# Kernel tuning notes

Hardware: AMD Instinct MI355X
Metric: run time of the kernel (lower is better)

## Reference

```python
import jax, jax.numpy as jnp
import numpy as np

N, IN_DIM, HID, E_DIM, E = 50000, 128, 256, 32, 400000
BN_INV = np.float32(1.0 / np.sqrt(1.0 + 1e-5))  # running_mean=0, running_var=1


def _lin_init(key, fan_in, fan_out):
    kw, kb = jax.random.split(key)
    s = 1.0 / np.sqrt(fan_in)
    W = jax.random.uniform(kw, (fan_in, fan_out), jnp.float32, -s, s)
    b = jax.random.uniform(kb, (fan_out,), jnp.float32, -s, s)
    return W, b


def setup_inputs() -> dict:
    key = jax.random.key(0)
    ks = jax.random.split(key, 12)
    x = jax.random.normal(ks[0], (N, IN_DIM), jnp.float32)
    edge_index = jax.random.randint(ks[1], (2, E), 0, N, jnp.int64)
    edge_attr = jax.random.normal(ks[2], (E, E_DIM), jnp.float32)
    Wn, bn_b = _lin_init(ks[3], IN_DIM, HID)
    We, be = _lin_init(ks[4], E_DIM, HID)
    Wa1, ba1 = _lin_init(ks[5], 2 * HID, HID)
    Wa2, ba2 = _lin_init(ks[6], HID, 1)
    W1, b1 = _lin_init(ks[7], HID, 2 * HID)
    W2, b2 = _lin_init(ks[8], 2 * HID, HID)
    gn = jnp.ones((HID,), jnp.float32); betan = jnp.zeros((HID,), jnp.float32)
    ge = jnp.ones((HID,), jnp.float32); betae = jnp.zeros((HID,), jnp.float32)
    gm = jnp.ones((2 * HID,), jnp.float32); betam = jnp.zeros((2 * HID,), jnp.float32)
    eps = jnp.zeros((1,), jnp.float32)
    return dict(x=x, edge_index=edge_index, edge_attr=edge_attr,
                Wn=Wn, bn_b=bn_b, gn=gn, betan=betan,
                We=We, be=be, ge=ge, betae=betae,
                Wa1=Wa1, ba1=ba1, Wa2=Wa2, ba2=ba2,
                W1=W1, b1=b1, gm=gm, betam=betam, W2=W2, b2=b2, eps=eps)


def _bn(h, g, b):
    # eval-mode BatchNorm1d with running_mean=0, running_var=1
    return h * (g * BN_INV) + b


def reference(x, edge_index, edge_attr, Wn, bn_b, gn, betan, We, be, ge, betae,
              Wa1, ba1, Wa2, ba2, W1, b1, gm, betam, W2, b2, eps):
    h = jax.nn.relu(_bn(x @ Wn + bn_b, gn, betan))           # [N, HID] node_encoder
    ef = jax.nn.relu(_bn(edge_attr @ We + be, ge, betae))    # [E, HID] edge_encoder
    row, col = edge_index[0], edge_index[1]
    ni = h[row]                                              # [E, HID]
    nj = h[col]                                              # [E, HID]
    att_in = jnp.concatenate([ni + ef, nj], axis=-1)         # [E, 2*HID]
    a = jnp.tanh(att_in @ Wa1 + ba1) @ Wa2 + ba2             # [E, 1]
    a = jax.nn.leaky_relu(a, 0.2)
    a = jax.nn.softmax(a, axis=0)                            # softmax over all edges
    msg = (nj + ef) * a                                      # [E, HID]
    agg = jnp.zeros_like(h).at[row].add(msg)                 # scatter-add
    out = (1.0 + eps) * h + agg
    mid = jax.nn.relu(_bn(out @ W1 + b1, gm, betam))         # MLP hidden [N, 2*HID]
    return mid @ W2 + b2                                     # [N, HID]
```

## Files before the change

kernel.cpp:

```cpp
#include <hip/hip_runtime.h>

typedef __attribute__((ext_vector_type(8))) short    s16x8;
typedef __attribute__((ext_vector_type(8))) unsigned short u16x8;
typedef __attribute__((ext_vector_type(4))) unsigned short u16x4;
typedef __attribute__((ext_vector_type(4))) float    f32x4;

#define BN_INV 0.9999950000374997f
#define MAXDEG 64
#define INV64  0.015625f

__device__ __forceinline__ unsigned short f2b(float f) {
    union { float f; unsigned u; } v; v.f = f;
    return (unsigned short)((v.u + 0x7FFFu + ((v.u >> 16) & 1u)) >> 16);
}
__device__ __forceinline__ float b2f(unsigned short b) {
    union { unsigned u; float f; } v; v.u = (unsigned)b << 16;
    return v.f;
}
__device__ __forceinline__ float fast_tanh(float x) {
    float e = __expf(-2.f * fabsf(x));
    float t = (1.f - e) / (1.f + e);
    return copysignf(t, x);
}

__global__ __launch_bounds__(256) void gemm_mfma(
    const void* __restrict__ Av, int lda, int a_f32,
    const unsigned short* __restrict__ BT, int ldb, int bsplit,
    float* __restrict__ Cf, unsigned short* __restrict__ Cb, int ldc,
    const float* __restrict__ bias, const float* __restrict__ gamma,
    const float* __restrict__ beta, int M, int K, int bnrelu)
{
    __shared__ unsigned short As[128 * 40];
    __shared__ unsigned short Bs[128 * 40];

    const int tid = threadIdx.x;
    const int row0 = blockIdx.y * 128;
    const int col0 = blockIdx.x * 128;
    const int w = tid >> 6, l = tid & 63;
    const int wr = (w >> 1) * 64;
    const int wc = (w & 1) * 64;
    const int srow = tid >> 1;
    const int shalf = (tid & 1) * 16;

    f32x4 acc[4][4];
    #pragma unroll
    for (int i = 0; i < 4; ++i)
        #pragma unroll
        for (int j = 0; j < 4; ++j)
            acc[i][j] = (f32x4){0.f, 0.f, 0.f, 0.f};

    const bool arow_ok = (row0 + srow) < M;
    const unsigned short* Ab = (const unsigned short*)Av + (size_t)(row0 + srow) * lda + shalf;
    const float*          Af = (const float*)Av          + (size_t)(row0 + srow) * lda + shalf;
    int bcol = col0 + srow, koff = 0;
    if (bsplit && col0 >= bsplit) { bcol -= bsplit; koff = bsplit; }
    const unsigned short* Bp = BT + (size_t)bcol * ldb + koff + shalf;

    const int lrow = (l >> 4) * 4;
    const int lcol = l & 15;
    const int kfrag = (l >> 4) * 8;

    for (int kt = 0; kt < K; kt += 32) {
        u16x8 av0 = {0, 0, 0, 0, 0, 0, 0, 0};
        u16x8 av1 = {0, 0, 0, 0, 0, 0, 0, 0};
        if (arow_ok) {
            if (a_f32) {
                float4 u0 = *(const float4*)(Af + kt);
                float4 u1 = *(const float4*)(Af + kt + 4);
                float4 u2 = *(const float4*)(Af + kt + 8);
                float4 u3 = *(const float4*)(Af + kt + 12);
                av0 = (u16x8){ f2b(u0.x), f2b(u0.y), f2b(u0.z), f2b(u0.w),
                               f2b(u1.x), f2b(u1.y), f2b(u1.z), f2b(u1.w) };
                av1 = (u16x8){ f2b(u2.x), f2b(u2.y), f2b(u2.z), f2b(u2.w),
                               f2b(u3.x), f2b(u3.y), f2b(u3.z), f2b(u3.w) };
            } else {
                av0 = *(const u16x8*)(Ab + kt);
                av1 = *(const u16x8*)(Ab + kt + 8);
            }
        }
        u16x8 bv0 = *(const u16x8*)(Bp + kt);
        u16x8 bv1 = *(const u16x8*)(Bp + kt + 8);
        *(u16x8*)&As[srow * 40 + shalf]     = av0;
        *(u16x8*)&As[srow * 40 + shalf + 8] = av1;
        *(u16x8*)&Bs[srow * 40 + shalf]     = bv0;
        *(u16x8*)&Bs[srow * 40 + shalf + 8] = bv1;
        __syncthreads();
        s16x8 af[4], bfr[4];
        #pragma unroll
        for (int i = 0; i < 4; ++i)
            af[i] = *(const s16x8*)&As[(wr + i * 16 + lcol) * 40 + kfrag];
        #pragma unroll
        for (int j = 0; j < 4; ++j)
            bfr[j] = *(const s16x8*)&Bs[(wc + j * 16 + lcol) * 40 + kfrag];
        #pragma unroll
        for (int i = 0; i < 4; ++i)
            #pragma unroll
            for (int j = 0; j < 4; ++j)
                acc[i][j] = __builtin_amdgcn_mfma_f32_16x16x32_bf16(
                    af[i], bfr[j], acc[i][j], 0, 0, 0);
        __syncthreads();
    }

    #pragma unroll
    for (int j = 0; j < 4; ++j) {
        const int col = col0 + wc + j * 16 + lcol;
        const float bi = bias ? bias[col] : 0.f;
        float g = 1.f, bt = 0.f;
        if (bnrelu) { g = gamma[col] * BN_INV; bt = beta[col]; }
        #pragma unroll
        for (int i = 0; i < 4; ++i) {
            const int r0 = row0 + wr + i * 16 + lrow;
            #pragma unroll
            for (int q = 0; q < 4; ++q) {
                const int rr = r0 + q;
                if (rr < M) {
                    float v = acc[i][j][q] + bi;
                    if (bnrelu) v = fmaxf(v * g + bt, 0.f);
                    if (Cf) Cf[(size_t)rr * ldc + col] = v;
                    if (Cb) Cb[(size_t)rr * ldc + col] = f2b(v);
                }
            }
        }
    }
}

__global__ __launch_bounds__(256) void fused_edge(
    const float* __restrict__ ea,
    const int* __restrict__ ei,
    const unsigned short* __restrict__ WeT,
    const unsigned char* __restrict__ Wa1T8,
    const unsigned short* __restrict__ HAB,
    const float* __restrict__ be, const float* __restrict__ ge,
    const float* __restrict__ betae, const float* __restrict__ ba1,
    const float* __restrict__ Wa2, const float* __restrict__ ba2,
    unsigned char* __restrict__ EF,
    float* __restrict__ es, float* __restrict__ Ssum, int E)
{
    __shared__ __align__(16) unsigned char smem[18432];
    unsigned short* As  = (unsigned short*)smem;
    unsigned char*  EFs = smem;
    int*   sIdx = (int*)(smem + 16384);
    float* sRed = (float*)(smem + 16896);

    const int tid = threadIdx.x;
    const int row0 = blockIdx.x * 64;
    const int w = tid >> 6, l = tid & 63;
    const int lgrp = l >> 4, lcol = l & 15;
    const int kfrag = lgrp * 8;
    const int wc = w * 64;

    {
        const int sr = tid >> 2, sk = (tid & 3) * 8;
        u16x8 av = {0, 0, 0, 0, 0, 0, 0, 0};
        if (row0 + sr < E) {
            const float* ap = ea + (size_t)(row0 + sr) * 32 + sk;
            float4 u0 = *(const float4*)ap, u1 = *(const float4*)(ap + 4);
            av = (u16x8){ f2b(u0.x), f2b(u0.y), f2b(u0.z), f2b(u0.w),
                          f2b(u1.x), f2b(u1.y), f2b(u1.z), f2b(u1.w) };
        }
        *(u16x8*)&As[sr * 40 + sk] = av;
        if (tid < 64)       sIdx[tid] = (row0 + tid < E) ? ei[row0 + tid] : 0;
        else if (tid < 128) sIdx[tid] = (row0 + tid - 64 < E) ? ei[E + row0 + tid - 64] : 0;
    }
    __syncthreads();

    f32x4 acc[4][4];
    #pragma unroll
    for (int i = 0; i < 4; ++i)
        #pragma unroll
        for (int j = 0; j < 4; ++j)
            acc[i][j] = (f32x4){0.f, 0.f, 0.f, 0.f};

    {
        s16x8 af[4], bfr[4];
        #pragma unroll
        for (int i = 0; i < 4; ++i)
            af[i] = *(const s16x8*)&WeT[(wc + i * 16 + lcol) * 32 + kfrag];
        #pragma unroll
        for (int j = 0; j < 4; ++j)
            bfr[j] = *(const s16x8*)&As[(j * 16 + lcol) * 40 + kfrag];
        #pragma unroll
        for (int i = 0; i < 4; ++i)
            #pragma unroll
            for (int j = 0; j < 4; ++j)
                acc[i][j] = __builtin_amdgcn_mfma_f32_16x16x32_bf16(
                    af[i], bfr[j], acc[i][j], 0, 0, 0);
    }
    __syncthreads();

    #pragma unroll
    for (int i = 0; i < 4; ++i) {
        const int ch0 = wc + i * 16 + lgrp * 4;
        float4 g4 = *(const float4*)(ge + ch0);
        float4 t4 = *(const float4*)(betae + ch0);
        float4 b4 = *(const float4*)(be + ch0);
        g4.x *= BN_INV; g4.y *= BN_INV; g4.z *= BN_INV; g4.w *= BN_INV;
        #pragma unroll
        for (int j = 0; j < 4; ++j) {
            const int edge = j * 16 + lcol;
            float v0 = fmaxf((acc[i][j][0] + b4.x) * g4.x + t4.x, 0.f);
            float v1 = fmaxf((acc[i][j][1] + b4.y) * g4.y + t4.y, 0.f);
            float v2 = fmaxf((acc[i][j][2] + b4.z) * g4.z + t4.z, 0.f);
            float v3 = fmaxf((acc[i][j][3] + b4.w) * g4.w + t4.w, 0.f);
            int pk = __builtin_amdgcn_cvt_pk_fp8_f32(v0, v1, 0, false);
            pk = __builtin_amdgcn_cvt_pk_fp8_f32(v2, v3, pk, true);
            *(unsigned*)&EFs[edge * 256 + ((((ch0 >> 3) ^ (edge & 7)) << 3) | (ch0 & 7))]
                = (unsigned)pk;
            acc[i][j] = (f32x4){0.f, 0.f, 0.f, 0.f};
        }
    }
    __syncthreads();

    for (int kt = 0; kt < 256; kt += 32) {
        long af8[4], bf8[4];
        const int kb = (kt + kfrag) >> 3;
        #pragma unroll
        for (int i = 0; i < 4; ++i) {
            const int edge = i * 16 + lcol;
            af8[i] = *(const long*)&EFs[edge * 256 + ((kb ^ (edge & 7)) << 3)];
        }
        #pragma unroll
        for (int j = 0; j < 4; ++j)
            bf8[j] = *(const long*)&Wa1T8[(size_t)(wc + j * 16 + lcol) * 256 + kt + kfrag];
        #pragma unroll
        for (int i = 0; i < 4; ++i)
            #pragma unroll
            for (int j = 0; j < 4; ++j)
                acc[i][j] = __builtin_amdgcn_mfma_f32_16x16x32_fp8_fp8(
                    af8[i], bf8[j], acc[i][j], 0, 0, 0);
    }

    {
        const int row = tid >> 2, cb = (tid & 3) * 64;
        if (row0 + row < E) {
            unsigned char* dst = EF + (size_t)(row0 + row) * 256 + cb;
            #pragma unroll
            for (int t2 = 0; t2 < 8; ++t2) {
                const int b = (cb >> 3) + t2;
                *(long*)(dst + t2 * 8)
                    = *(const long*)&EFs[row * 256 + ((b ^ (row & 7)) << 3)];
            }
        }
    }

    {
        int colv[4]; float ba1c[4], wa2c[4];
        #pragma unroll
        for (int j = 0; j < 4; ++j) {
            colv[j] = wc + j * 16 + lcol;
            ba1c[j] = ba1[colv[j]];
            wa2c[j] = Wa2[colv[j]];
        }
        #pragma unroll
        for (int i = 0; i < 4; ++i) {
            #pragma unroll
            for (int q = 0; q < 4; ++q) {
                const int row = i * 16 + lgrp * 4 + q;
                const unsigned short* hap = HAB + (size_t)sIdx[row] * 512;
                const unsigned short* hbp = HAB + (size_t)sIdx[64 + row] * 512 + 256;
                float s = 0.f;
                #pragma unroll
                for (int j = 0; j < 4; ++j) {
                    float t = fast_tanh(fmaf(acc[i][j][q], INV64,
                                             b2f(hap[colv[j]]) + b2f(hbp[colv[j]]) + ba1c[j]));
                    s += t * wa2c[j];
                }
                s += __shfl_xor(s, 1); s += __shfl_xor(s, 2);
                s += __shfl_xor(s, 4); s += __shfl_xor(s, 8);
                if (lcol == 0) sRed[row * 4 + w] = s;
            }
        }
    }
    __syncthreads();

    if (tid < 64) {
        const int ge = row0 + tid;
        float sv = sRed[tid * 4] + sRed[tid * 4 + 1]
                 + sRed[tid * 4 + 2] + sRed[tid * 4 + 3] + ba2[0];
        sv = sv > 0.f ? sv : 0.2f * sv;
        float ev = __expf(sv);
        float contrib = 0.f;
        if (ge < E) { es[ge] = ev; contrib = ev; }
        #pragma unroll
        for (int off = 32; off; off >>= 1) contrib += __shfl_xor(contrib, off);
        if (l == 0) atomicAdd(Ssum, contrib);
    }
}

__global__ __launch_bounds__(256) void fill_kernel(
    const int* __restrict__ ei, int* __restrict__ cnt, int* __restrict__ perm,
    int E)
{
    int e = blockIdx.x * 256 + threadIdx.x;
    const int stride = gridDim.x * 256;
    for (; e < E; e += stride) {
        const int r = ei[e];
        const int pos = atomicAdd(&cnt[r], 1);
        if (pos < MAXDEG) perm[(size_t)r * MAXDEG + pos] = e;
    }
}

__global__ __launch_bounds__(256) void gather_kernel(
    const int* __restrict__ ei, const unsigned char* __restrict__ EF,
    const unsigned short* __restrict__ h_bf, const float* __restrict__ es,
    const int* __restrict__ cnt, const int* __restrict__ perm,
    const float* __restrict__ eps, const float* __restrict__ Ssum,
    unsigned short* __restrict__ ob_bf, int N, int E)
{
    const int w = threadIdx.x >> 6, l = threadIdx.x & 63;
    const int r = blockIdx.x * 4 + w;
    if (r >= N) return;
    const int k0 = l * 4;

    const int deg = cnt[r] < MAXDEG ? cnt[r] : MAXDEG;
    const int pe = perm[(size_t)r * MAXDEG + l];
    const float esl = (l < deg) ? es[pe] : 0.f;
    const int   cl  = (l < deg) ? ei[E + pe] : 0;

    f32x4 acc = {0.f, 0.f, 0.f, 0.f};
    u16x4 hv_c = {0, 0, 0, 0}; int ef_c = 0; float es_c = 0.f;
    if (deg > 0) {
        const int e0 = __shfl(pe, 0), c0 = __shfl(cl, 0);
        es_c = __shfl(esl, 0);
        hv_c = *(const u16x4*)(h_bf + (size_t)c0 * 256 + k0);
        ef_c = *(const int*)(EF + (size_t)e0 * 256 + k0);
    }
    for (int p = 0; p < deg; ++p) {
        u16x4 hv_n = {0, 0, 0, 0}; int ef_n = 0; float es_n = 0.f;
        if (p + 1 < deg) {
            const int en = __shfl(pe, p + 1), cn = __shfl(cl, p + 1);
            es_n = __shfl(esl, p + 1);
            hv_n = *(const u16x4*)(h_bf + (size_t)cn * 256 + k0);
            ef_n = *(const int*)(EF + (size_t)en * 256 + k0);
        }
        acc[0] += es_c * (b2f(hv_c[0]) + __builtin_amdgcn_cvt_f32_fp8(ef_c, 0));
        acc[1] += es_c * (b2f(hv_c[1]) + __builtin_amdgcn_cvt_f32_fp8(ef_c, 1));
        acc[2] += es_c * (b2f(hv_c[2]) + __builtin_amdgcn_cvt_f32_fp8(ef_c, 2));
        acc[3] += es_c * (b2f(hv_c[3]) + __builtin_amdgcn_cvt_f32_fp8(ef_c, 3));
        hv_c = hv_n; ef_c = ef_n; es_c = es_n;
    }

    const float sc = 1.f + eps[0];
    const float invS = 1.f / Ssum[0];
    u16x4 hr = *(const u16x4*)(h_bf + (size_t)r * 256 + k0);
    u16x4 o = { f2b(sc * b2f(hr[0]) + acc[0] * invS),
                f2b(sc * b2f(hr[1]) + acc[1] * invS),
                f2b(sc * b2f(hr[2]) + acc[2] * invS),
                f2b(sc * b2f(hr[3]) + acc[3] * invS) };
    *(u16x4*)(ob_bf + (size_t)r * 256 + k0) = o;
}

__global__ __launch_bounds__(256) void prep_kernel(
    const float* __restrict__ Wn, const float* __restrict__ We,
    const float* __restrict__ Wa1, const float* __restrict__ W1,
    const float* __restrict__ W2,
    unsigned short* __restrict__ WnT, unsigned short* __restrict__ WeT,
    unsigned short* __restrict__ Wa1T, unsigned char* __restrict__ Wa1T8,
    unsigned short* __restrict__ W1T, unsigned short* __restrict__ W2T,
    int* __restrict__ cnt, float* __restrict__ Ssum, int N)
{
    const int b = blockIdx.x, t = threadIdx.x;
    { const int i = b * 256 + t; if (i < N) cnt[i] = 0; }
    if (b == 0 && t == 0) Ssum[0] = 0.f;
    if (b < 128) {
        WnT[t * 128 + b] = f2b(Wn[(size_t)b * 256 + t]);
    } else if (b < 160) {
        const int rr = b - 128;
        WeT[t * 32 + rr] = f2b(We[(size_t)rr * 256 + t]);
    } else if (b < 672) {
        const int rr = b - 160;
        const float v = Wa1[(size_t)rr * 256 + t];
        Wa1T[t * 512 + rr] = f2b(v);
        if (rr < 256) {
            int pk = __builtin_amdgcn_cvt_pk_fp8_f32(v * 64.f, 0.f, 0, false);
            Wa1T8[(size_t)t * 256 + rr] = (unsigned char)(pk & 0xFF);
        }
    } else if (b < 928) {
        const int rr = b - 672;
        W1T[(size_t)t * 256 + rr]         = f2b(W1[(size_t)rr * 512 + t]);
        W1T[(size_t)(t + 256) * 256 + rr] = f2b(W1[(size_t)rr * 512 + t + 256]);
    } else if (b < 1440) {
        const int rr = b - 928;
        W2T[(size_t)t * 512 + rr] = f2b(W2[(size_t)rr * 256 + t]);
    }
}

extern "C" void kernel_launch(void* const* d_in, const int* in_sizes, int n_in,
                              void* d_out, int out_size, void* d_ws, size_t ws_size,
                              hipStream_t stream)
{
    const float* x     = (const float*)d_in[0];
    const int*   ei    = (const int*)  d_in[1];
    const float* eattr = (const float*)d_in[2];
    const float* Wn    = (const float*)d_in[3];
    const float* bnb   = (const float*)d_in[4];
    const float* gn    = (const float*)d_in[5];
    const float* betan = (const float*)d_in[6];
    const float* We    = (const float*)d_in[7];
    const float* be    = (const float*)d_in[8];
    const float* ge    = (const float*)d_in[9];
    const float* betae = (const float*)d_in[10];
    const float* Wa1   = (const float*)d_in[11];
    const float* ba1   = (const float*)d_in[12];
    const float* Wa2   = (const float*)d_in[13];
    const float* ba2   = (const float*)d_in[14];
    const float* W1    = (const float*)d_in[15];
    const float* b1    = (const float*)d_in[16];
    const float* gm    = (const float*)d_in[17];
    const float* betam = (const float*)d_in[18];
    const float* W2    = (const float*)d_in[19];
    const float* b2    = (const float*)d_in[20];
    const float* eps   = (const float*)d_in[21];

    const int N = in_sizes[0] / 128;
    const int E = in_sizes[1] / 2;

    char* p = (char*)d_ws;
    auto alloc = [&](size_t bytes) {
        char* r = p; p += (bytes + 255) & ~(size_t)255; return r;
    };
    unsigned char*  EF    = (unsigned char*) alloc((size_t)E * 256);
    unsigned short* h_bf  = (unsigned short*)alloc((size_t)N * 256 * 2);
    unsigned short* HAB   = (unsigned short*)alloc((size_t)N * 512 * 2);
    float*          es    = (float*)         alloc((size_t)E * 4);
    int*            cnt   = (int*)            alloc((size_t)N * 4);
    int*            perm  = (int*)            alloc((size_t)N * MAXDEG * 4);
    float*          Ssum  = (float*)         alloc(256);
    unsigned short* WnT   = (unsigned short*)alloc(256 * 128 * 2);
    unsigned short* WeT   = (unsigned short*)alloc(256 * 32 * 2);
    unsigned short* Wa1T  = (unsigned short*)alloc(256 * 512 * 2);
    unsigned char*  Wa1T8 = (unsigned char*) alloc(256 * 256);
    unsigned short* W1T   = (unsigned short*)alloc(512 * 256 * 2);
    unsigned short* W2T   = (unsigned short*)alloc(256 * 512 * 2);
    unsigned short* ob_bf = HAB;
    unsigned short* mid   = (unsigned short*)EF;

    dim3 blk(256);
    const int rbN = (N + 127) / 128;

    prep_kernel<<<1440, blk, 0, stream>>>(Wn, We, Wa1, W1, W2,
        WnT, WeT, Wa1T, Wa1T8, W1T, W2T, cnt, Ssum, N);
    fill_kernel<<<512, blk, 0, stream>>>(ei, cnt, perm, E);

    gemm_mfma<<<dim3(2, rbN), blk, 0, stream>>>(x, 128, 1, WnT, 128, 0,
        nullptr, h_bf, 256, bnb, gn, betan, N, 128, 1);
    gemm_mfma<<<dim3(4, rbN), blk, 0, stream>>>(h_bf, 256, 0, Wa1T, 512, 256,
        nullptr, HAB, 512, nullptr, nullptr, nullptr, N, 256, 0);

    fused_edge<<<(E + 63) / 64, blk, 0, stream>>>(
        eattr, ei, WeT, Wa1T8, HAB, be, ge, betae, ba1, Wa2, ba2,
        EF, es, Ssum, E);

    gather_kernel<<<(N + 3) / 4, blk, 0, stream>>>(ei, EF, h_bf, es,
        cnt, perm, eps, Ssum, ob_bf, N, E);

    gemm_mfma<<<dim3(4, rbN), blk, 0, stream>>>(ob_bf, 256, 0, W1T, 256, 0,
        nullptr, mid, 512, b1, gm, betam, N, 256, 1);
    gemm_mfma<<<dim3(2, rbN), blk, 0, stream>>>(mid, 512, 0, W2T, 512, 0,
        (float*)d_out, nullptr, 256, b2, nullptr, nullptr, N, 512, 0);
}
```

Baseline: 534.5 us.

## Fuse consecutive GEMM pairs into one kernel keeping the intermediate tile in LDS

Two consecutive GEMMs are merged into a single kernel that works on 32-row blocks. The first GEMM's bias, BN and ReLU output goes to shared memory as bf16 and feeds the second GEMM straight from there. This fuses the node-encoder GEMM with the attention projection, and W1 with W2 in the final MLP. It removes the global round trip of the [N,512] intermediate and one read of h, and cuts the launch count. In exchange, each block reads whole weight matrices from global or L2 with no LDS reuse across rows, which may raise cache traffic and lower MFMA efficiency compared with the old 128x128 tiled GEMM.

```diff
diff --git a/kernel.cpp b/kernel.cpp
--- a/kernel.cpp
+++ b/kernel.cpp
@@ -23,101 +23,134 @@
     return copysignf(t, x);
 }
 
-__global__ __launch_bounds__(256) void gemm_mfma(
+__global__ __launch_bounds__(256) void fused_mlp(
     const void* __restrict__ Av, int lda, int a_f32,
-    const unsigned short* __restrict__ BT, int ldb, int bsplit,
-    float* __restrict__ Cf, unsigned short* __restrict__ Cb, int ldc,
-    const float* __restrict__ bias, const float* __restrict__ gamma,
-    const float* __restrict__ beta, int M, int K, int bnrelu)
-{
-    __shared__ unsigned short As[128 * 40];
-    __shared__ unsigned short Bs[128 * 40];
-
+    const unsigned short* __restrict__ B1T,
+    const float* __restrict__ bias1, const float* __restrict__ g1,
+    const float* __restrict__ bt1,
+    const unsigned short* __restrict__ B2T, int ldb2, int bsplit2,
+    const float* __restrict__ bias2,
+    unsigned short* __restrict__ Tout,
+    float* __restrict__ Of, unsigned short* __restrict__ Ob,
+    int M, int K1, int N1, int N2)
+{
+    __shared__ unsigned short T[32 * 520];
     const int tid = threadIdx.x;
-    const int row0 = blockIdx.y * 128;
-    const int col0 = blockIdx.x * 128;
+    const int row0 = blockIdx.x * 32;
     const int w = tid >> 6, l = tid & 63;
-    const int wr = (w >> 1) * 64;
-    const int wc = (w & 1) * 64;
-    const int srow = tid >> 1;
-    const int shalf = (tid & 1) * 16;
-
-    f32x4 acc[4][4];
-    #pragma unroll
-    for (int i = 0; i < 4; ++i)
-        #pragma unroll
-        for (int j = 0; j < 4; ++j)
-            acc[i][j] = (f32x4){0.f, 0.f, 0.f, 0.f};
-
-    const bool arow_ok = (row0 + srow) < M;
-    const unsigned short* Ab = (const unsigned short*)Av + (size_t)(row0 + srow) * lda + shalf;
-    const float*          Af = (const float*)Av          + (size_t)(row0 + srow) * lda + shalf;
-    int bcol = col0 + srow, koff = 0;
-    if (bsplit && col0 >= bsplit) { bcol -= bsplit; koff = bsplit; }
-    const unsigned short* Bp = BT + (size_t)bcol * ldb + koff + shalf;
-
-    const int lrow = (l >> 4) * 4;
-    const int lcol = l & 15;
-    const int kfrag = (l >> 4) * 8;
-
-    for (int kt = 0; kt < K; kt += 32) {
-        u16x8 av0 = {0, 0, 0, 0, 0, 0, 0, 0};
-        u16x8 av1 = {0, 0, 0, 0, 0, 0, 0, 0};
-        if (arow_ok) {
-            if (a_f32) {
-                float4 u0 = *(const float4*)(Af + kt);
-                float4 u1 = *(const float4*)(Af + kt + 4);
-                float4 u2 = *(const float4*)(Af + kt + 8);
-                float4 u3 = *(const float4*)(Af + kt + 12);
-                av0 = (u16x8){ f2b(u0.x), f2b(u0.y), f2b(u0.z), f2b(u0.w),
-                               f2b(u1.x), f2b(u1.y), f2b(u1.z), f2b(u1.w) };
-                av1 = (u16x8){ f2b(u2.x), f2b(u2.y), f2b(u2.z), f2b(u2.w),
-                               f2b(u3.x), f2b(u3.y), f2b(u3.z), f2b(u3.w) };
-            } else {
-                av0 = *(const u16x8*)(Ab + kt);
-                av1 = *(const u16x8*)(Ab + kt + 8);
-            }
-        }
-        u16x8 bv0 = *(const u16x8*)(Bp + kt);
-        u16x8 bv1 = *(const u16x8*)(Bp + kt + 8);
-        *(u16x8*)&As[srow * 40 + shalf]     = av0;
-        *(u16x8*)&As[srow * 40 + shalf + 8] = av1;
-        *(u16x8*)&Bs[srow * 40 + shalf]     = bv0;
-        *(u16x8*)&Bs[srow * 40 + shalf + 8] = bv1;
-        __syncthreads();
-        s16x8 af[4], bfr[4];
-        #pragma unroll
-        for (int i = 0; i < 4; ++i)
-            af[i] = *(const s16x8*)&As[(wr + i * 16 + lcol) * 40 + kfrag];
-        #pragma unroll
-        for (int j = 0; j < 4; ++j)
-            bfr[j] = *(const s16x8*)&Bs[(wc + j * 16 + lcol) * 40 + kfrag];
-        #pragma unroll
-        for (int i = 0; i < 4; ++i)
+    const int lgrp = l >> 4, lcol = l & 15;
+    const int kfrag = lgrp * 8;
+
+    for (int c0 = 0; c0 < N1; c0 += 256) {
+        const int wcol = c0 + w * 64;
+        f32x4 acc[4][2];
+        #pragma unroll
+        for (int i = 0; i < 4; ++i) {
+            acc[i][0] = (f32x4){0.f, 0.f, 0.f, 0.f};
+            acc[i][1] = (f32x4){0.f, 0.f, 0.f, 0.f};
+        }
+        for (int kt = 0; kt < K1; kt += 32) {
+            s16x8 af[4], bfr[2];
+            #pragma unroll
+            for (int i = 0; i < 4; ++i)
+                af[i] = *(const s16x8*)&B1T[(size_t)(wcol + i * 16 + lcol) * K1 + kt + kfrag];
+            #pragma unroll
+            for (int j = 0; j < 2; ++j) {
+                const int r = row0 + j * 16 + lcol;
+                u16x8 bv = {0, 0, 0, 0, 0, 0, 0, 0};
+                if (r < M) {
+                    if (a_f32) {
+                        const float* ap = (const float*)Av + (size_t)r * lda + kt + kfrag;
+                        float4 u0 = *(const float4*)ap, u1 = *(const float4*)(ap + 4);
+                        bv = (u16x8){ f2b(u0.x), f2b(u0.y), f2b(u0.z), f2b(u0.w),
+                                      f2b(u1.x), f2b(u1.y), f2b(u1.z), f2b(u1.w) };
+                    } else {
+                        bv = *(const u16x8*)((const unsigned short*)Av + (size_t)r * lda + kt + kfrag);
+                    }
+                }
+                bfr[j] = (s16x8)bv;
+            }
+            #pragma unroll
+            for (int i = 0; i < 4; ++i)
+                #pragma unroll
+                for (int j = 0; j < 2; ++j)
+                    acc[i][j] = __builtin_amdgcn_mfma_f32_16x16x32_bf16(
+                        af[i], bfr[j], acc[i][j], 0, 0, 0);
+        }
+        #pragma unroll
+        for (int i = 0; i < 4; ++i) {
+            const int cq = wcol + i * 16 + lgrp * 4;
+            float4 b4 = *(const float4*)(bias1 + cq);
+            float4 g4 = *(const float4*)(g1 + cq);
+            float4 t4 = *(const float4*)(bt1 + cq);
+            g4.x *= BN_INV; g4.y *= BN_INV; g4.z *= BN_INV; g4.w *= BN_INV;
+            #pragma unroll
+            for (int j = 0; j < 2; ++j) {
+                const int r = j * 16 + lcol;
+                u16x4 pk = { f2b(fmaxf((acc[i][j][0] + b4.x) * g4.x + t4.x, 0.f)),
+                             f2b(fmaxf((acc[i][j][1] + b4.y) * g4.y + t4.y, 0.f)),
+                             f2b(fmaxf((acc[i][j][2] + b4.z) * g4.z + t4.z, 0.f)),
+                             f2b(fmaxf((acc[i][j][3] + b4.w) * g4.w + t4.w, 0.f)) };
+                *(u16x4*)&T[r * 520 + cq] = pk;
+            }
+        }
+    }
+    __syncthreads();
+
+    if (Tout) {
+        const int r = tid >> 3, cs = (tid & 7) * 32;
+        if (row0 + r < M) {
+            #pragma unroll
+            for (int t2 = 0; t2 < 4; ++t2) {
+                u16x8 v = *(const u16x8*)&T[r * 520 + cs + t2 * 8];
+                *(u16x8*)&Tout[(size_t)(row0 + r) * 256 + cs + t2 * 8] = v;
+            }
+        }
+    }
+
+    for (int c0 = 0; c0 < N2; c0 += 256) {
+        const int wcol = c0 + w * 64;
+        f32x4 acc2[2][4];
+        #pragma unroll
+        for (int i = 0; i < 2; ++i)
             #pragma unroll
             for (int j = 0; j < 4; ++j)
-                acc[i][j] = __builtin_amdgcn_mfma_f32_16x16x32_bf16(
-                    af[i], bfr[j], acc[i][j], 0, 0, 0);
-        __syncthreads();
-    }
-
-    #pragma unroll
-    for (int j = 0; j < 4; ++j) {
-        const int col = col0 + wc + j * 16 + lcol;
-        const float bi = bias ? bias[col] : 0.f;
-        float g = 1.f, bt = 0.f;
-        if (bnrelu) { g = gamma[col] * BN_INV; bt = beta[col]; }
-        #pragma unroll
-        for (int i = 0; i < 4; ++i) {
-            const int r0 = row0 + wr + i * 16 + lrow;
-            #pragma unroll
-            for (int q = 0; q < 4; ++q) {
-                const int rr = r0 + q;
-                if (rr < M) {
-                    float v = acc[i][j][q] + bi;
-                    if (bnrelu) v = fmaxf(v * g + bt, 0.f);
-                    if (Cf) Cf[(size_t)rr * ldc + col] = v;
-                    if (Cb) Cb[(size_t)rr * ldc + col] = f2b(v);
+                acc2[i][j] = (f32x4){0.f, 0.f, 0.f, 0.f};
+        for (int kt = 0; kt < N1; kt += 32) {
+            s16x8 af2[2], bf2[4];
+            #pragma unroll
+            for (int i = 0; i < 2; ++i)
+                af2[i] = *(const s16x8*)&T[(i * 16 + lcol) * 520 + kt + kfrag];
+            #pragma unroll
+            for (int j = 0; j < 4; ++j) {
+                const int c = wcol + j * 16 + lcol;
+                const size_t base = (bsplit2 && c >= bsplit2)
+                    ? (size_t)(c - bsplit2) * ldb2 + bsplit2
+                    : (size_t)c * ldb2;
+                bf2[j] = *(const s16x8*)&B2T[base + kt + kfrag];
+            }
+            #pragma unroll
+            for (int i = 0; i < 2; ++i)
+                #pragma unroll
+                for (int j = 0; j < 4; ++j)
+                    acc2[i][j] = __builtin_amdgcn_mfma_f32_16x16x32_bf16(
+                        af2[i], bf2[j], acc2[i][j], 0, 0, 0);
+        }
+        #pragma unroll
+        for (int j = 0; j < 4; ++j) {
+            const int c = wcol + j * 16 + lcol;
+            const float bi = bias2 ? bias2[c] : 0.f;
+            #pragma unroll
+            for (int i = 0; i < 2; ++i) {
+                const int r0q = row0 + i * 16 + lgrp * 4;
+                #pragma unroll
+                for (int q = 0; q < 4; ++q) {
+                    const int rr = r0q + q;
+                    if (rr < M) {
+                        float v = acc2[i][j][q] + bi;
+                        if (Of) Of[(size_t)rr * N2 + c] = v;
+                        else    Ob[(size_t)rr * N2 + c] = f2b(v);
+                    }
                 }
             }
         }
@@ -433,19 +466,16 @@
     unsigned short* W1T   = (unsigned short*)alloc(512 * 256 * 2);
     unsigned short* W2T   = (unsigned short*)alloc(256 * 512 * 2);
     unsigned short* ob_bf = HAB;
-    unsigned short* mid   = (unsigned short*)EF;
 
     dim3 blk(256);
-    const int rbN = (N + 127) / 128;
+    const int rbN32 = (N + 31) / 32;
 
     prep_kernel<<<1440, blk, 0, stream>>>(Wn, We, Wa1, W1, W2,
         WnT, WeT, Wa1T, Wa1T8, W1T, W2T, cnt, Ssum, N);
     fill_kernel<<<512, blk, 0, stream>>>(ei, cnt, perm, E);
 
-    gemm_mfma<<<dim3(2, rbN), blk, 0, stream>>>(x, 128, 1, WnT, 128, 0,
-        nullptr, h_bf, 256, bnb, gn, betan, N, 128, 1);
-    gemm_mfma<<<dim3(4, rbN), blk, 0, stream>>>(h_bf, 256, 0, Wa1T, 512, 256,
-        nullptr, HAB, 512, nullptr, nullptr, nullptr, N, 256, 0);
+    fused_mlp<<<rbN32, blk, 0, stream>>>(x, 128, 1, WnT, bnb, gn, betan,
+        Wa1T, 512, 256, nullptr, h_bf, nullptr, HAB, N, 128, 256, 512);
 
     fused_edge<<<(E + 63) / 64, blk, 0, stream>>>(
         eattr, ei, WeT, Wa1T8, HAB, be, ge, betae, ba1, Wa2, ba2,
@@ -454,8 +484,6 @@
     gather_kernel<<<(N + 3) / 4, blk, 0, stream>>>(ei, EF, h_bf, es,
         cnt, perm, eps, Ssum, ob_bf, N, E);
 
-    gemm_mfma<<<dim3(4, rbN), blk, 0, stream>>>(ob_bf, 256, 0, W1T, 256, 0,
-        nullptr, mid, 512, b1, gm, betam, N, 256, 1);
-    gemm_mfma<<<dim3(2, rbN), blk, 0, stream>>>(mid, 512, 0, W2T, 512, 0,
-        (float*)d_out, nullptr, 256, b2, nullptr, nullptr, N, 512, 0);
-}
+    fused_mlp<<<rbN32, blk, 0, stream>>>(ob_bf, 256, 0, W1T, b1, gm, betam,
+        W2T, 512, 0, b2, nullptr, (float*)d_out, nullptr, N, 256, 512, 256);
+}
```

New measurement: 560.9 us. +4.9%, slower.

## Split fused_edge across 8 waves with 32 output channels each

Applied to the files above, without the earlier changes.

The fused edge kernel now runs 512 threads per block instead of 256. Each of the 8 waves owns 32 output channels instead of 64, so per-wave accumulators shrink from 16 to 8 MFMA tiles, and the staging, store and score-reduction loops are re-indexed to match. The aim is lower register pressure and more waves in flight to hide the gather and global loads. The cost is redundant per-wave loads of the shared EF fragments, a larger 8-way shared-memory reduction, and bigger blocks that may limit occupancy in other ways.

```diff
diff --git a/kernel.cpp b/kernel.cpp
--- a/kernel.cpp
+++ b/kernel.cpp
@@ -124,7 +124,7 @@
     }
 }
 
-__global__ __launch_bounds__(256) void fused_edge(
+__global__ __launch_bounds__(512) void fused_edge(
     const float* __restrict__ ea,
     const int* __restrict__ ei,
     const unsigned short* __restrict__ WeT,
@@ -136,7 +136,7 @@
     unsigned char* __restrict__ EF,
     float* __restrict__ es, float* __restrict__ Ssum, int E)
 {
-    __shared__ __align__(16) unsigned char smem[18432];
+    __shared__ __align__(16) unsigned char smem[18944];
     unsigned short* As  = (unsigned short*)smem;
     unsigned char*  EFs = smem;
     int*   sIdx = (int*)(smem + 16384);
@@ -147,49 +147,47 @@
     const int w = tid >> 6, l = tid & 63;
     const int lgrp = l >> 4, lcol = l & 15;
     const int kfrag = lgrp * 8;
-    const int wc = w * 64;
+    const int wc = w * 32;
 
     {
-        const int sr = tid >> 2, sk = (tid & 3) * 8;
-        u16x8 av = {0, 0, 0, 0, 0, 0, 0, 0};
+        const int sr = tid >> 3, sk = (tid & 7) * 4;
+        u16x4 av = {0, 0, 0, 0};
         if (row0 + sr < E) {
             const float* ap = ea + (size_t)(row0 + sr) * 32 + sk;
-            float4 u0 = *(const float4*)ap, u1 = *(const float4*)(ap + 4);
-            av = (u16x8){ f2b(u0.x), f2b(u0.y), f2b(u0.z), f2b(u0.w),
-                          f2b(u1.x), f2b(u1.y), f2b(u1.z), f2b(u1.w) };
-        }
-        *(u16x8*)&As[sr * 40 + sk] = av;
+            float4 u0 = *(const float4*)ap;
+            av = (u16x4){ f2b(u0.x), f2b(u0.y), f2b(u0.z), f2b(u0.w) };
+        }
+        *(u16x4*)&As[sr * 40 + sk] = av;
         if (tid < 64)       sIdx[tid] = (row0 + tid < E) ? ei[row0 + tid] : 0;
         else if (tid < 128) sIdx[tid] = (row0 + tid - 64 < E) ? ei[E + row0 + tid - 64] : 0;
     }
     __syncthreads();
 
-    f32x4 acc[4][4];
+    f32x4 a1[2][4];
     #pragma unroll
-    for (int i = 0; i < 4; ++i)
+    for (int i = 0; i < 2; ++i)
         #pragma unroll
         for (int j = 0; j < 4; ++j)
-            acc[i][j] = (f32x4){0.f, 0.f, 0.f, 0.f};
-
+            a1[i][j] = (f32x4){0.f, 0.f, 0.f, 0.f};
     {
-        s16x8 af[4], bfr[4];
-        #pragma unroll
-        for (int i = 0; i < 4; ++i)
+        s16x8 af[2], bfr[4];
+        #pragma unroll
+        for (int i = 0; i < 2; ++i)
             af[i] = *(const s16x8*)&WeT[(wc + i * 16 + lcol) * 32 + kfrag];
         #pragma unroll
         for (int j = 0; j < 4; ++j)
             bfr[j] = *(const s16x8*)&As[(j * 16 + lcol) * 40 + kfrag];
         #pragma unroll
-        for (int i = 0; i < 4; ++i)
+        for (int i = 0; i < 2; ++i)
             #pragma unroll
             for (int j = 0; j < 4; ++j)
-                acc[i][j] = __builtin_amdgcn_mfma_f32_16x16x32_bf16(
-                    af[i], bfr[j], acc[i][j], 0, 0, 0);
+                a1[i][j] = __builtin_amdgcn_mfma_f32_16x16x32_bf16(
+                    af[i], bfr[j], a1[i][j], 0, 0, 0);
     }
     __syncthreads();
 
     #pragma unroll
-    for (int i = 0; i < 4; ++i) {
+    for (int i = 0; i < 2; ++i) {
         const int ch0 = wc + i * 16 + lgrp * 4;
         float4 g4 = *(const float4*)(ge + ch0);
         float4 t4 = *(const float4*)(betae + ch0);
@@ -198,21 +196,26 @@
         #pragma unroll
         for (int j = 0; j < 4; ++j) {
             const int edge = j * 16 + lcol;
-            float v0 = fmaxf((acc[i][j][0] + b4.x) * g4.x + t4.x, 0.f);
-            float v1 = fmaxf((acc[i][j][1] + b4.y) * g4.y + t4.y, 0.f);
-            float v2 = fmaxf((acc[i][j][2] + b4.z) * g4.z + t4.z, 0.f);
-            float v3 = fmaxf((acc[i][j][3] + b4.w) * g4.w + t4.w, 0.f);
+            float v0 = fmaxf((a1[i][j][0] + b4.x) * g4.x + t4.x, 0.f);
+            float v1 = fmaxf((a1[i][j][1] + b4.y) * g4.y + t4.y, 0.f);
+            float v2 = fmaxf((a1[i][j][2] + b4.z) * g4.z + t4.z, 0.f);
+            float v3 = fmaxf((a1[i][j][3] + b4.w) * g4.w + t4.w, 0.f);
             int pk = __builtin_amdgcn_cvt_pk_fp8_f32(v0, v1, 0, false);
             pk = __builtin_amdgcn_cvt_pk_fp8_f32(v2, v3, pk, true);
             *(unsigned*)&EFs[edge * 256 + ((((ch0 >> 3) ^ (edge & 7)) << 3) | (ch0 & 7))]
                 = (unsigned)pk;
-            acc[i][j] = (f32x4){0.f, 0.f, 0.f, 0.f};
         }
     }
     __syncthreads();
 
+    f32x4 a2[4][2];
+    #pragma unroll
+    for (int i = 0; i < 4; ++i)
+        #pragma unroll
+        for (int j = 0; j < 2; ++j)
+            a2[i][j] = (f32x4){0.f, 0.f, 0.f, 0.f};
     for (int kt = 0; kt < 256; kt += 32) {
-        long af8[4], bf8[4];
+        long af8[4], bf8[2];
         const int kb = (kt + kfrag) >> 3;
         #pragma unroll
         for (int i = 0; i < 4; ++i) {
@@ -220,22 +223,22 @@
             af8[i] = *(const long*)&EFs[edge * 256 + ((kb ^ (edge & 7)) << 3)];
         }
         #pragma unroll
-        for (int j = 0; j < 4; ++j)
+        for (int j = 0; j < 2; ++j)
             bf8[j] = *(const long*)&Wa1T8[(size_t)(wc + j * 16 + lcol) * 256 + kt + kfrag];
         #pragma unroll
         for (int i = 0; i < 4; ++i)
             #pragma unroll
-            for (int j = 0; j < 4; ++j)
-                acc[i][j] = __builtin_amdgcn_mfma_f32_16x16x32_fp8_fp8(
-                    af8[i], bf8[j], acc[i][j], 0, 0, 0);
+            for (int j = 0; j < 2; ++j)
+                a2[i][j] = __builtin_amdgcn_mfma_f32_16x16x32_fp8_fp8(
+                    af8[i], bf8[j], a2[i][j], 0, 0, 0);
     }
 
     {
-        const int row = tid >> 2, cb = (tid & 3) * 64;
+        const int row = tid >> 3, cb = (tid & 7) * 32;
         if (row0 + row < E) {
             unsigned char* dst = EF + (size_t)(row0 + row) * 256 + cb;
             #pragma unroll
-            for (int t2 = 0; t2 < 8; ++t2) {
+            for (int t2 = 0; t2 < 4; ++t2) {
                 const int b = (cb >> 3) + t2;
                 *(long*)(dst + t2 * 8)
                     = *(const long*)&EFs[row * 256 + ((b ^ (row & 7)) << 3)];
@@ -244,9 +247,9 @@
     }
 
     {
-        int colv[4]; float ba1c[4], wa2c[4];
-        #pragma unroll
-        for (int j = 0; j < 4; ++j) {
+        int colv[2]; float ba1c[2], wa2c[2];
+        #pragma unroll
+        for (int j = 0; j < 2; ++j) {
             colv[j] = wc + j * 16 + lcol;
             ba1c[j] = ba1[colv[j]];
             wa2c[j] = Wa2[colv[j]];
@@ -260,14 +263,14 @@
                 const unsigned short* hbp = HAB + (size_t)sIdx[64 + row] * 512 + 256;
                 float s = 0.f;
                 #pragma unroll
-                for (int j = 0; j < 4; ++j) {
-                    float t = fast_tanh(fmaf(acc[i][j][q], INV64,
+                for (int j = 0; j < 2; ++j) {
+                    float t = fast_tanh(fmaf(a2[i][j][q], INV64,
                                              b2f(hap[colv[j]]) + b2f(hbp[colv[j]]) + ba1c[j]));
                     s += t * wa2c[j];
                 }
                 s += __shfl_xor(s, 1); s += __shfl_xor(s, 2);
                 s += __shfl_xor(s, 4); s += __shfl_xor(s, 8);
-                if (lcol == 0) sRed[row * 4 + w] = s;
+                if (lcol == 0) sRed[row * 8 + w] = s;
             }
         }
     }
@@ -275,8 +278,9 @@
 
     if (tid < 64) {
         const int ge = row0 + tid;
-        float sv = sRed[tid * 4] + sRed[tid * 4 + 1]
-                 + sRed[tid * 4 + 2] + sRed[tid * 4 + 3] + ba2[0];
+        float sv = ba2[0];
+        #pragma unroll
+        for (int t2 = 0; t2 < 8; ++t2) sv += sRed[tid * 8 + t2];
         sv = sv > 0.f ? sv : 0.2f * sv;
         float ev = __expf(sv);
         float contrib = 0.f;
@@ -447,7 +451,7 @@
     gemm_mfma<<<dim3(4, rbN), blk, 0, stream>>>(h_bf, 256, 0, Wa1T, 512, 256,
         nullptr, HAB, 512, nullptr, nullptr, nullptr, N, 256, 0);
 
-    fused_edge<<<(E + 63) / 64, blk, 0, stream>>>(
+    fused_edge<<<(E + 63) / 64, dim3(512), 0, stream>>>(
         eattr, ei, WeT, Wa1T8, HAB, be, ge, betae, ba1, Wa2, ba2,
         EF, es, Ssum, E);
 
```

Result: no change. 525.8 us (-1.6%).
